# Kernel optimization log

Hardware: AMD Instinct MI355X
Metric: run time of the kernel (lower is better)

Reference implementation:

```python
import jax, jax.numpy as jnp
import numpy as np

N = 8192
IN_DIM = 256
OUT_DIM = 256
NEG_INF = -1000000000.0
LEAKY_SLOPE = 0.2


def setup_inputs() -> dict:
    key = jax.random.key(0)
    k_h, k_adj, k_W, k_a = jax.random.split(key, 4)
    h = jax.random.normal(k_h, (N, IN_DIM), dtype=jnp.float32)
    adj = jax.random.randint(k_adj, (N, N), 0, 2, dtype=jnp.int32)
    # learned params (nn.Linear without bias stores weight [out, in]; we keep [in, out] for x @ W)
    W = jax.random.normal(k_W, (IN_DIM, OUT_DIM), dtype=jnp.float32) / np.sqrt(IN_DIM)
    a = jax.random.normal(k_a, (OUT_DIM,), dtype=jnp.float32) / np.sqrt(OUT_DIM)
    return {"h": h, "adj": adj, "W": W, "a": a}


def reference(h, adj, W, a):
    Wh = h @ W                                   # [N, out_dim]
    f = Wh @ a                                   # [N]
    e = jax.nn.leaky_relu(f[:, None] + f[None, :], LEAKY_SLOPE)  # [N, N]
    mask = (adj > 0).astype(Wh.dtype)
    e_masked = e * mask + (1.0 - mask) * NEG_INF
    alpha = jax.nn.softmax(e_masked, axis=1)     # [N, N]
    h_prime = alpha @ Wh                         # [N, out_dim]
    return jax.nn.elu(h_prime), alpha
```

## Files before the change

### kernel.cpp

```cpp
#include <hip/hip_runtime.h>
#include <hip/hip_bf16.h>

#define NROW 8192
#define DIM 256

typedef short bf16x8 __attribute__((ext_vector_type(8)));
typedef float f32x4 __attribute__((ext_vector_type(4)));

__device__ __forceinline__ short f2bf(float x) {
    return __builtin_bit_cast(short, __float2bfloat16(x));
}

__device__ __forceinline__ void gload_lds16(const void* g, void* l) {
    __builtin_amdgcn_global_load_lds(
        (const __attribute__((address_space(1))) unsigned int*)g,
        (__attribute__((address_space(3))) unsigned int*)l, 16, 0, 0);
}

__global__ __launch_bounds__(256) void k1_whgemm(
    const float* __restrict__ h, const float* __restrict__ W,
    const float* __restrict__ a, short* __restrict__ whbT,
    float* __restrict__ f)
{
    __shared__ float hs[64][65];
    __shared__ float wsm[64][65];
    const int tid = threadIdx.x;
    const int tx = tid & 15, ty = tid >> 4;
    const int i0 = blockIdx.x * 64;
    const int n0 = blockIdx.y * 64;

    float acc[4][4];
#pragma unroll
    for (int u = 0; u < 4; ++u)
#pragma unroll
        for (int v = 0; v < 4; ++v) acc[u][v] = 0.f;

    for (int kb = 0; kb < DIM; kb += 64) {
#pragma unroll
        for (int rr = 0; rr < 4; ++rr) {
            int row = rr * 16 + ty;
            *(float4*)&hs[row][tx * 4] =
                *(const float4*)&h[(size_t)(i0 + row) * DIM + kb + tx * 4];
            *(float4*)&wsm[row][tx * 4] =
                *(const float4*)&W[(size_t)(kb + row) * DIM + n0 + tx * 4];
        }
        __syncthreads();
#pragma unroll 8
        for (int kk = 0; kk < 64; ++kk) {
            float av[4], bv[4];
#pragma unroll
            for (int u = 0; u < 4; ++u) av[u] = hs[ty * 4 + u][kk];
#pragma unroll
            for (int v = 0; v < 4; ++v) bv[v] = wsm[kk][tx * 4 + v];
#pragma unroll
            for (int u = 0; u < 4; ++u)
#pragma unroll
                for (int v = 0; v < 4; ++v) acc[u][v] += av[u] * bv[v];
        }
        __syncthreads();
    }

#pragma unroll
    for (int u = 0; u < 4; ++u)
#pragma unroll
        for (int v = 0; v < 4; ++v) hs[ty * 4 + u][tx * 4 + v] = acc[u][v];
    __syncthreads();

    {
        int r = tid >> 2, q = tid & 3;
        float s = 0.f;
#pragma unroll
        for (int c = 0; c < 16; ++c) s += hs[r][q * 16 + c] * a[n0 + q * 16 + c];
        s += __shfl_xor(s, 1);
        s += __shfl_xor(s, 2);
        if (q == 0) atomicAdd(&f[i0 + r], s);
    }

    {
        int n = tid >> 2, q = tid & 3;
        union { short s[16]; int4 i4[2]; } pk;
#pragma unroll
        for (int b = 0; b < 4; ++b)
#pragma unroll
            for (int c = 0; c < 4; ++c)
                pk.s[b * 4 + c] = f2bf(hs[q * 16 + b * 4 + c][n]);
        size_t base = ((size_t)(i0 >> 6) * 256 + n0 + n) * 64 + q * 16;
        *(int4*)&whbT[base] = pk.i4[0];
        *(int4*)&whbT[base + 8] = pk.i4[1];
    }
}

__global__ __launch_bounds__(256) void k3c_alpha(
    const int* __restrict__ adj, const float* __restrict__ f,
    float* __restrict__ alpha)
{
    const int i = blockIdx.x;
    const int tid = threadIdx.x;
    const float fi = f[i];
    const int* row = adj + (size_t)i * NROW;

    float4 tv[8];
    float sum = 0.f;
#pragma unroll
    for (int it = 0; it < 8; ++it) {
        const int j = it * 1024 + tid * 4;
        int4 av = *(const int4*)&row[j];
        float4 fv = *(const float4*)&f[j];
        float x0 = fi + fv.x, x1 = fi + fv.y, x2 = fi + fv.z, x3 = fi + fv.w;
        float4 t;
        t.x = av.x > 0 ? __expf(fmaxf(x0, 0.2f * x0)) : 0.f;
        t.y = av.y > 0 ? __expf(fmaxf(x1, 0.2f * x1)) : 0.f;
        t.z = av.z > 0 ? __expf(fmaxf(x2, 0.2f * x2)) : 0.f;
        t.w = av.w > 0 ? __expf(fmaxf(x3, 0.2f * x3)) : 0.f;
        tv[it] = t;
        sum += t.x + t.y + t.z + t.w;
    }

#pragma unroll
    for (int off = 32; off > 0; off >>= 1) sum += __shfl_xor(sum, off);
    __shared__ float red[4];
    if ((tid & 63) == 0) red[tid >> 6] = sum;
    __syncthreads();
    const float inv = 1.f / (red[0] + red[1] + red[2] + red[3]);

    float* arow = alpha + (size_t)i * NROW;
#pragma unroll
    for (int it = 0; it < 8; ++it) {
        float4 t = tv[it];
        float4 o = {t.x * inv, t.y * inv, t.z * inv, t.w * inv};
        *(float4*)&arow[it * 1024 + tid * 4] = o;
    }
}

__global__ __launch_bounds__(512) void k4d_gemm(
    const float* __restrict__ alpha, const short* __restrict__ whbT,
    float* __restrict__ out0)
{
    __shared__ __align__(16) short Bs[2][16384];

    const int tid = threadIdx.x;
    const int wave = tid >> 6;
    const int lane = tid & 63;
    const int lo = lane & 15;
    const int quad = lane >> 4;
    const int q8 = quad * 8;
    const int rg = wave & 1;
    const int cg = wave >> 1;
    const int i0 = blockIdx.x * 32;

    const float* aptr = alpha + (size_t)(i0 + rg * 16 + lo) * NROW + q8;

    const int srow = lane >> 3;
    const int swz = ((lane & 7) ^ srow) * 8;

    const int bx0 = (quad ^ (lo & 7)) * 8;
    const int bx1 = ((4 + quad) ^ (lo & 7)) * 8;
    int off0[4], off1[4];
#pragma unroll
    for (int nt = 0; nt < 4; ++nt) {
        int rb = (cg * 64 + nt * 16 + lo) * 64;
        off0[nt] = rb + bx0;
        off1[nt] = rb + bx1;
    }

    f32x4 acc[4] = {};
    float4 na0, na1, na2, na3;

#define STAGE(buf, kt)                                                        \
    {                                                                         \
        const short* gtile = whbT + (size_t)(kt) * 16384;                     \
        _Pragma("unroll")                                                     \
        for (int s = 0; s < 4; ++s) {                                         \
            gload_lds16(gtile + ((wave * 4 + s) * 8 + srow) * 64 + swz,       \
                        &Bs[buf][(wave * 4 + s) * 512]);                      \
        }                                                                     \
    }

#define KBODY(buf, kt, DOSTAGE)                                               \
    {                                                                         \
        if (DOSTAGE) STAGE((buf) ^ 1, (kt) + 1);                              \
        const float4 ca0 = na0, ca1 = na1, ca2 = na2, ca3 = na3;              \
        if (DOSTAGE) {                                                        \
            const float* ap = aptr + (size_t)((kt) + 1) * 64;                 \
            na0 = *(const float4*)ap;                                         \
            na1 = *(const float4*)(ap + 4);                                   \
            na2 = *(const float4*)(ap + 32);                                  \
            na3 = *(const float4*)(ap + 36);                                  \
        }                                                                     \
        bf16x8 af0, af1;                                                      \
        af0[0] = f2bf(ca0.x); af0[1] = f2bf(ca0.y);                           \
        af0[2] = f2bf(ca0.z); af0[3] = f2bf(ca0.w);                           \
        af0[4] = f2bf(ca1.x); af0[5] = f2bf(ca1.y);                           \
        af0[6] = f2bf(ca1.z); af0[7] = f2bf(ca1.w);                           \
        af1[0] = f2bf(ca2.x); af1[1] = f2bf(ca2.y);                           \
        af1[2] = f2bf(ca2.z); af1[3] = f2bf(ca2.w);                           \
        af1[4] = f2bf(ca3.x); af1[5] = f2bf(ca3.y);                           \
        af1[6] = f2bf(ca3.z); af1[7] = f2bf(ca3.w);                           \
        _Pragma("unroll")                                                     \
        for (int nt = 0; nt < 4; ++nt) {                                      \
            bf16x8 b0 = *(const bf16x8*)&Bs[buf][off0[nt]];                   \
            acc[nt] = __builtin_amdgcn_mfma_f32_16x16x32_bf16(af0, b0,        \
                                                          acc[nt], 0, 0, 0);  \
            bf16x8 b1 = *(const bf16x8*)&Bs[buf][off1[nt]];                   \
            acc[nt] = __builtin_amdgcn_mfma_f32_16x16x32_bf16(af1, b1,        \
                                                          acc[nt], 0, 0, 0);  \
        }                                                                     \
        asm volatile("s_waitcnt vmcnt(0)" ::: "memory");                      \
        __syncthreads();                                                      \
    }

    STAGE(0, 0);
    na0 = *(const float4*)aptr;
    na1 = *(const float4*)(aptr + 4);
    na2 = *(const float4*)(aptr + 32);
    na3 = *(const float4*)(aptr + 36);
    asm volatile("s_waitcnt vmcnt(0)" ::: "memory");
    __syncthreads();

#pragma unroll 1
    for (int kt = 0; kt < 126; kt += 2) {
        KBODY(0, kt, true)
        KBODY(1, kt + 1, true)
    }
    KBODY(0, 126, true)
    KBODY(1, 127, false)

#undef STAGE
#undef KBODY

    const int ccb = cg * 64 + lo;
#pragma unroll
    for (int nt = 0; nt < 4; ++nt) {
#pragma unroll
        for (int c = 0; c < 4; ++c) {
            const int rr = i0 + rg * 16 + quad * 4 + c;
            float v = acc[nt][c];
            v = v > 0.f ? v : __expf(v) - 1.f;
            out0[(size_t)rr * DIM + ccb + nt * 16] = v;
        }
    }
}

extern "C" void kernel_launch(void* const* d_in, const int* in_sizes, int n_in,
                              void* d_out, int out_size, void* d_ws, size_t ws_size,
                              hipStream_t stream) {
    const float* h = (const float*)d_in[0];
    const int* adj = (const int*)d_in[1];
    const float* W = (const float*)d_in[2];
    const float* a = (const float*)d_in[3];
    float* out0 = (float*)d_out;
    float* alpha = out0 + (size_t)NROW * DIM;

    char* ws = (char*)d_ws;
    float* f = (float*)ws;
    short* whbT = (short*)(ws + 32768);

    hipMemsetAsync(f, 0, NROW * sizeof(float), stream);
    k1_whgemm<<<dim3(NROW / 64, DIM / 64), 256, 0, stream>>>(h, W, a, whbT, f);
    k3c_alpha<<<dim3(NROW), 256, 0, stream>>>(adj, f, alpha);
    k4d_gemm<<<dim3(NROW / 32), 512, 0, stream>>>(alpha, whbT, out0);
}
```

Before: 713.7 us.

## Deepen alpha-GEMM pipeline to four LDS buffers with counted vmcnt waits

Reworks the alpha @ Wh GEMM kernel from a double-buffered loop into a 4-slot ring that prefetches two k-tiles ahead. Both the B-tile LDS loads and the alpha register loads are issued two steps early through inline asm. A partial s_waitcnt vmcnt(16) plus s_barrier replaces the full vmcnt(0) drain before every step, so memory latency can overlap compute. LDS use doubles to 128KB per block and the launch bound asks for 2 blocks per CU, so register pressure and occupancy limits may now constrain the kernel.

```diff
diff --git a/kernel.cpp b/kernel.cpp
--- a/kernel.cpp
+++ b/kernel.cpp
@@ -132,11 +132,11 @@
     }
 }
 
-__global__ __launch_bounds__(512) void k4d_gemm(
+__global__ __launch_bounds__(512, 2) void k4e_gemm(
     const float* __restrict__ alpha, const short* __restrict__ whbT,
     float* __restrict__ out0)
 {
-    __shared__ __align__(16) short Bs[2][16384];
+    __shared__ __align__(16) short Bs[4][16384];
 
     const int tid = threadIdx.x;
     const int wave = tid >> 6;
@@ -164,69 +164,86 @@
     }
 
     f32x4 acc[4] = {};
-    float4 na0, na1, na2, na3;
+    f32x4 aA[4], aB[4], aC[4], aD[4];
 
 #define STAGE(buf, kt)                                                        \
     {                                                                         \
         const short* gtile = whbT + (size_t)(kt) * 16384;                     \
         _Pragma("unroll")                                                     \
-        for (int s = 0; s < 4; ++s) {                                         \
+        for (int s = 0; s < 4; ++s)                                           \
             gload_lds16(gtile + ((wave * 4 + s) * 8 + srow) * 64 + swz,       \
                         &Bs[buf][(wave * 4 + s) * 512]);                      \
-        }                                                                     \
-    }
-
-#define KBODY(buf, kt, DOSTAGE)                                               \
-    {                                                                         \
-        if (DOSTAGE) STAGE((buf) ^ 1, (kt) + 1);                              \
-        const float4 ca0 = na0, ca1 = na1, ca2 = na2, ca3 = na3;              \
-        if (DOSTAGE) {                                                        \
-            const float* ap = aptr + (size_t)((kt) + 1) * 64;                 \
-            na0 = *(const float4*)ap;                                         \
-            na1 = *(const float4*)(ap + 4);                                   \
-            na2 = *(const float4*)(ap + 32);                                  \
-            na3 = *(const float4*)(ap + 36);                                  \
-        }                                                                     \
+    }
+
+#define ALOAD(set, kt)                                                        \
+    {                                                                         \
+        const float* ap = aptr + (size_t)(kt) * 64;                           \
+        asm volatile("global_load_dwordx4 %0, %4, off\n\t"                    \
+                     "global_load_dwordx4 %1, %4, off offset:16\n\t"          \
+                     "global_load_dwordx4 %2, %4, off offset:128\n\t"         \
+                     "global_load_dwordx4 %3, %4, off offset:144"             \
+                     : "=&v"(aA[set]), "=&v"(aB[set]),                        \
+                       "=&v"(aC[set]), "=&v"(aD[set])                         \
+                     : "v"(ap));                                              \
+    }
+
+#define CONSUME(c)                                                            \
+    {                                                                         \
         bf16x8 af0, af1;                                                      \
-        af0[0] = f2bf(ca0.x); af0[1] = f2bf(ca0.y);                           \
-        af0[2] = f2bf(ca0.z); af0[3] = f2bf(ca0.w);                           \
-        af0[4] = f2bf(ca1.x); af0[5] = f2bf(ca1.y);                           \
-        af0[6] = f2bf(ca1.z); af0[7] = f2bf(ca1.w);                           \
-        af1[0] = f2bf(ca2.x); af1[1] = f2bf(ca2.y);                           \
-        af1[2] = f2bf(ca2.z); af1[3] = f2bf(ca2.w);                           \
-        af1[4] = f2bf(ca3.x); af1[5] = f2bf(ca3.y);                           \
-        af1[6] = f2bf(ca3.z); af1[7] = f2bf(ca3.w);                           \
+        af0[0] = f2bf(aA[c][0]); af0[1] = f2bf(aA[c][1]);                     \
+        af0[2] = f2bf(aA[c][2]); af0[3] = f2bf(aA[c][3]);                     \
+        af0[4] = f2bf(aB[c][0]); af0[5] = f2bf(aB[c][1]);                     \
+        af0[6] = f2bf(aB[c][2]); af0[7] = f2bf(aB[c][3]);                     \
+        af1[0] = f2bf(aC[c][0]); af1[1] = f2bf(aC[c][1]);                     \
+        af1[2] = f2bf(aC[c][2]); af1[3] = f2bf(aC[c][3]);                     \
+        af1[4] = f2bf(aD[c][0]); af1[5] = f2bf(aD[c][1]);                     \
+        af1[6] = f2bf(aD[c][2]); af1[7] = f2bf(aD[c][3]);                     \
         _Pragma("unroll")                                                     \
         for (int nt = 0; nt < 4; ++nt) {                                      \
-            bf16x8 b0 = *(const bf16x8*)&Bs[buf][off0[nt]];                   \
+            bf16x8 b0 = *(const bf16x8*)&Bs[c][off0[nt]];                     \
             acc[nt] = __builtin_amdgcn_mfma_f32_16x16x32_bf16(af0, b0,        \
                                                           acc[nt], 0, 0, 0);  \
-            bf16x8 b1 = *(const bf16x8*)&Bs[buf][off1[nt]];                   \
+            bf16x8 b1 = *(const bf16x8*)&Bs[c][off1[nt]];                     \
             acc[nt] = __builtin_amdgcn_mfma_f32_16x16x32_bf16(af1, b1,        \
                                                           acc[nt], 0, 0, 0);  \
         }                                                                     \
-        asm volatile("s_waitcnt vmcnt(0)" ::: "memory");                      \
-        __syncthreads();                                                      \
-    }
-
-    STAGE(0, 0);
-    na0 = *(const float4*)aptr;
-    na1 = *(const float4*)(aptr + 4);
-    na2 = *(const float4*)(aptr + 32);
-    na3 = *(const float4*)(aptr + 36);
+    }
+
+#define KSTEP_FULL(kt, c)                                                     \
+    {                                                                         \
+        STAGE(((c) + 2) & 3, (kt) + 2);                                       \
+        ALOAD(((c) + 2) & 3, (kt) + 2);                                       \
+        asm volatile("s_waitcnt vmcnt(16)" ::: "memory");                     \
+        __builtin_amdgcn_s_barrier();                                         \
+        __builtin_amdgcn_sched_barrier(0);                                    \
+        CONSUME(c)                                                            \
+    }
+
+    STAGE(0, 0); ALOAD(0, 0);
+    STAGE(1, 1); ALOAD(1, 1);
+
+#pragma unroll 1
+    for (int base = 0; base < 124; base += 4) {
+        KSTEP_FULL(base + 0, 0)
+        KSTEP_FULL(base + 1, 1)
+        KSTEP_FULL(base + 2, 2)
+        KSTEP_FULL(base + 3, 3)
+    }
+    KSTEP_FULL(124, 0)
+    KSTEP_FULL(125, 1)
+    asm volatile("s_waitcnt vmcnt(8)" ::: "memory");
+    __builtin_amdgcn_s_barrier();
+    __builtin_amdgcn_sched_barrier(0);
+    CONSUME(2)
     asm volatile("s_waitcnt vmcnt(0)" ::: "memory");
-    __syncthreads();
-
-#pragma unroll 1
-    for (int kt = 0; kt < 126; kt += 2) {
-        KBODY(0, kt, true)
-        KBODY(1, kt + 1, true)
-    }
-    KBODY(0, 126, true)
-    KBODY(1, 127, false)
+    __builtin_amdgcn_s_barrier();
+    __builtin_amdgcn_sched_barrier(0);
+    CONSUME(3)
 
 #undef STAGE
-#undef KBODY
+#undef ALOAD
+#undef CONSUME
+#undef KSTEP_FULL
 
     const int ccb = cg * 64 + lo;
 #pragma unroll
@@ -258,5 +275,5 @@
     hipMemsetAsync(f, 0, NROW * sizeof(float), stream);
     k1_whgemm<<<dim3(NROW / 64, DIM / 64), 256, 0, stream>>>(h, W, a, whbT, f);
     k3c_alpha<<<dim3(NROW), 256, 0, stream>>>(adj, f, alpha);
-    k4d_gemm<<<dim3(NROW / 32), 512, 0, stream>>>(alpha, whbT, out0);
-}
+    k4e_gemm<<<dim3(NROW / 32), 512, 0, stream>>>(alpha, whbT, out0);
+}
```

Result: faster. 654.7 us (-8.3%).
